# Kernel tuning notes

Measured on AMD Instinct MI355X. Metric: run time of the kernel, lower is better.

Reference implementation:

```python
import jax, jax.numpy as jnp
import numpy as np

B, N, D = 256, 50, 128
NEG = -9e15  # torch uses -9000000000000000.0
LEAKY_SLOPE = 0.2


def setup_inputs() -> dict:
    key = jax.random.key(0)
    ks = jax.random.split(key, 6)
    hidden = jax.random.normal(ks[0], (B, N, D), dtype=jnp.float32)
    adj = jax.random.randint(ks[1], (B, N, N), 0, 5)  # edge types 0..4
    a_0 = jax.random.normal(ks[2], (D, 1), dtype=jnp.float32) * 0.05
    a_1 = jax.random.normal(ks[3], (D, 1), dtype=jnp.float32) * 0.05
    a_2 = jax.random.normal(ks[4], (D, 1), dtype=jnp.float32) * 0.05
    a_3 = jax.random.normal(ks[5], (D, 1), dtype=jnp.float32) * 0.05
    return {"hidden": hidden, "adj": adj, "a_0": a_0, "a_1": a_1, "a_2": a_2, "a_3": a_3}


def reference(hidden, adj, a_0, a_1, a_2, a_3):
    # LocalAggregator.forward (typed-edge GAT over session graph).
    # Original builds a_input[b,i,j,:] = h[b,i,:]*h[b,j,:] (B,N,N,D) then
    # projects with 4 relation vectors a_k (D,1). We fuse: stack the 4
    # vectors and contract D in one einsum -> e[b,k,i,j].
    A = jnp.concatenate([a_0, a_1, a_2, a_3], axis=1)          # (D, 4)
    e = jnp.einsum('bid,bjd,dk->bkij', hidden, hidden, A)      # (B, 4, N, N)
    e = jax.nn.leaky_relu(e, negative_slope=LEAKY_SLOPE)
    # Per-edge-type masking: adj value v in {1..4} selects branch v-1,
    # anything else gets -9e15 (same chained torch.where semantics/order).
    scores = jnp.full_like(e[:, 0], NEG)                        # (B, N, N)
    scores = jnp.where(adj == 1, e[:, 0], scores)
    scores = jnp.where(adj == 2, e[:, 1], scores)
    scores = jnp.where(adj == 3, e[:, 2], scores)
    scores = jnp.where(adj == 4, e[:, 3], scores)
    attn = jax.nn.softmax(scores, axis=-1)                      # (B, N, N)
    return jnp.einsum('bij,bjd->bid', attn, hidden)             # (B, N, D)
```

## Files before the change

### kernel.cpp

```cpp
#include <hip/hip_runtime.h>
#include <stdint.h>

typedef __attribute__((ext_vector_type(8))) short short8;
typedef __attribute__((ext_vector_type(4))) float f32x4;

namespace {
constexpr int   kN     = 50;
constexpr int   kD     = 128;
constexpr float kNeg   = -9.0e15f;
constexpr float kSlope = 0.2f;
constexpr int   HS16   = 136;
constexpr int   ADS    = 52;
constexpr int   HTW    = 66;
constexpr int   PW     = 72;
}

union Pack8 { uint32_t u[4]; short8 s; };

__device__ __forceinline__ uint32_t pack_hl(float v) {
    const uint32_t b  = __float_as_uint(v);
    const uint32_t hi = b & 0xffff0000u;
    const float    r  = v - __uint_as_float(hi);
    return (b >> 16) | (__float_as_uint(r) & 0xffff0000u);
}

__global__ __launch_bounds__(512)
void gat_v13_kernel(const float* __restrict__ hidden,
                    const int*   __restrict__ adj,
                    const float* __restrict__ a0,
                    const float* __restrict__ a1,
                    const float* __restrict__ a2,
                    const float* __restrict__ a3,
                    float* __restrict__ out)
{
    __shared__ unsigned short Hhi[64 * HS16];
    __shared__ unsigned short Hlo[64 * HS16];
    __shared__ uint32_t       Hti[128 * HTW];
    __shared__ unsigned char  Ad [kN * ADS];
    __shared__ float          Xch[8][64][16];
    __shared__ unsigned short Pw2[8][16 * PW];

    const int b    = blockIdx.x;
    const int tid  = threadIdx.x;
    const int lane = tid & 63;
    const int wid  = __builtin_amdgcn_readfirstlane(tid >> 6);
    const int g    = lane >> 4;
    const int f    = lane & 15;

    const float* __restrict__ hb   = hidden + (size_t)b * (kN * kD);
    const int*   __restrict__ adjb = adj    + (size_t)b * (kN * kN);
    float*       __restrict__ outb = out    + (size_t)b * (kN * kD);

    const float4* hg = reinterpret_cast<const float4*>(hb);
    #pragma unroll
    for (int it4 = 0; it4 < 4; ++it4) {
        const int idx = tid + it4 * 512;
        const int j   = idx >> 5;
        const int d4  = idx & 31;
        float4 v = make_float4(0.f, 0.f, 0.f, 0.f);
        if (j < kN) v = hg[j * 32 + d4];

        const uint32_t h0 = __float_as_uint(v.x) & 0xffff0000u;
        const uint32_t h1 = __float_as_uint(v.y) & 0xffff0000u;
        const uint32_t h2 = __float_as_uint(v.z) & 0xffff0000u;
        const uint32_t h3 = __float_as_uint(v.w) & 0xffff0000u;
        uint2 hiw;
        hiw.x = h1 | (h0 >> 16);
        hiw.y = h3 | (h2 >> 16);
        const float r0 = v.x - __uint_as_float(h0);
        const float r1 = v.y - __uint_as_float(h1);
        const float r2 = v.z - __uint_as_float(h2);
        const float r3 = v.w - __uint_as_float(h3);
        uint2 low;
        low.x = (__float_as_uint(r1) & 0xffff0000u) | (__float_as_uint(r0) >> 16);
        low.y = (__float_as_uint(r3) & 0xffff0000u) | (__float_as_uint(r2) >> 16);
        *reinterpret_cast<uint2*>(&Hhi[j * HS16 + 4 * d4]) = hiw;
        *reinterpret_cast<uint2*>(&Hlo[j * HS16 + 4 * d4]) = low;
    }
    for (int idx = tid; idx < 625; idx += 512) {
        const int4 v = reinterpret_cast<const int4*>(adjb)[idx];
        const int e = 4 * idx;
        const int vv[4] = {v.x, v.y, v.z, v.w};
        #pragma unroll
        for (int p = 0; p < 4; ++p) {
            const int ee  = e + p;
            const int row = ee / kN;
            const int col = ee - kN * row;
            Ad[row * ADS + col] = (unsigned char)vv[p];
        }
    }
    const float2* hb2 = reinterpret_cast<const float2*>(hb);
    float2 tv0[4], tv1[4];
    #pragma unroll
    for (int it4 = 0; it4 < 4; ++it4) {
        const int jp = wid + 8 * it4;
        const int j0 = 2 * jp, j1 = 2 * jp + 1;
        tv0[it4] = (j0 < kN) ? hb2[j0 * 64 + lane] : make_float2(0.f, 0.f);
        tv1[it4] = (j1 < kN) ? hb2[j1 * 64 + lane] : make_float2(0.f, 0.f);
    }
    __syncthreads();

    const int it   = wid & 3;
    const int kh   = wid >> 2;
    const int i0   = 16 * it;
    const int irow = (i0 + f < kN) ? (i0 + f) : (kN - 1);

    int adv[4][4];
    #pragma unroll
    for (int jt = 0; jt < 4; ++jt) {
        const int j = 16 * jt + f;
        #pragma unroll
        for (int reg = 0; reg < 4; ++reg) {
            const int ii  = i0 + 4 * g + reg;
            const int iic = (ii < kN) ? ii : (kN - 1);
            adv[jt][reg] = (j < kN) ? (int)Ad[iic * ADS + j] : 0;
        }
    }

    f32x4 acc[4][4];
    #pragma unroll
    for (int jt = 0; jt < 4; ++jt)
        #pragma unroll
        for (int k = 0; k < 4; ++k) acc[jt][k] = (f32x4){0.f, 0.f, 0.f, 0.f};

    const float* __restrict__ aks[4] = {a0, a1, a2, a3};

    #pragma unroll
    for (int ksl2 = 0; ksl2 < 2; ++ksl2) {
        const int dofs = 64 * kh + 32 * ksl2 + 8 * g;

        const short8 ah8 = *reinterpret_cast<const short8*>(&Hhi[irow * HS16 + dofs]);
        const short8 al8 = *reinterpret_cast<const short8*>(&Hlo[irow * HS16 + dofs]);
        float ha[8];
        #pragma unroll
        for (int p = 0; p < 8; ++p) {
            const uint32_t uh = ((uint32_t)(unsigned short)ah8[p]) << 16;
            const uint32_t ul = ((uint32_t)(unsigned short)al8[p]) << 16;
            ha[p] = __uint_as_float(uh) + __uint_as_float(ul);
        }

        short8 qh[4], ql[4];
        #pragma unroll
        for (int k = 0; k < 4; ++k) {
            const float4 av0 = *reinterpret_cast<const float4*>(aks[k] + dofs);
            const float4 av1 = *reinterpret_cast<const float4*>(aks[k] + dofs + 4);
            const float aa[8] = {av0.x, av0.y, av0.z, av0.w, av1.x, av1.y, av1.z, av1.w};
            Pack8 ph, pl;
            #pragma unroll
            for (int p = 0; p < 4; ++p) {
                const float q0 = ha[2 * p]     * aa[2 * p];
                const float q1 = ha[2 * p + 1] * aa[2 * p + 1];
                const uint32_t b0 = __float_as_uint(q0) & 0xffff0000u;
                const uint32_t b1 = __float_as_uint(q1) & 0xffff0000u;
                ph.u[p] = b1 | (b0 >> 16);
                const float s0 = q0 - __uint_as_float(b0);
                const float s1 = q1 - __uint_as_float(b1);
                pl.u[p] = (__float_as_uint(s1) & 0xffff0000u) | (__float_as_uint(s0) >> 16);
            }
            qh[k] = ph.s;
            ql[k] = pl.s;
        }

        #pragma unroll
        for (int jt = 0; jt < 4; ++jt) {
            const int jrow = 16 * jt + f;
            const short8 bh = *reinterpret_cast<const short8*>(&Hhi[jrow * HS16 + dofs]);
            const short8 bl = *reinterpret_cast<const short8*>(&Hlo[jrow * HS16 + dofs]);
            #pragma unroll
            for (int k = 0; k < 4; ++k) {
                acc[jt][k] = __builtin_amdgcn_mfma_f32_16x16x32_bf16(qh[k], bh, acc[jt][k], 0, 0, 0);
                acc[jt][k] = __builtin_amdgcn_mfma_f32_16x16x32_bf16(qh[k], bl, acc[jt][k], 0, 0, 0);
                acc[jt][k] = __builtin_amdgcn_mfma_f32_16x16x32_bf16(ql[k], bh, acc[jt][k], 0, 0, 0);
            }
        }
    }

    f32x4 spart[4];
    uint32_t vmask = 0;
    #pragma unroll
    for (int jt = 0; jt < 4; ++jt) {
        #pragma unroll
        for (int reg = 0; reg < 4; ++reg) {
            const int kv = adv[jt][reg];
            const bool valid = (kv >= 1) && (kv <= 4);
            spart[jt][reg] = (kv == 1) ? acc[jt][0][reg]
                           : (kv == 2) ? acc[jt][1][reg]
                           : (kv == 3) ? acc[jt][2][reg]
                           : (kv == 4) ? acc[jt][3][reg] : 0.f;
            vmask |= (valid ? 1u : 0u) << (4 * jt + reg);
        }
    }

    #pragma unroll
    for (int it4 = 0; it4 < 4; ++it4) {
        const int jp = wid + 8 * it4;
        const int j0 = 2 * jp;
        const int d2 = lane;
        uint2 wa, wb;
        wa.x = pack_hl(tv0[it4].x); wa.y = pack_hl(tv1[it4].x);
        wb.x = pack_hl(tv0[it4].y); wb.y = pack_hl(tv1[it4].y);
        *reinterpret_cast<uint2*>(&Hti[(2 * d2 + 0) * HTW + j0]) = wa;
        *reinterpret_cast<uint2*>(&Hti[(2 * d2 + 1) * HTW + j0]) = wb;
    }

    #pragma unroll
    for (int jt = 0; jt < 4; ++jt)
        *reinterpret_cast<f32x4*>(&Xch[wid][lane][4 * jt]) = spart[jt];
    __syncthreads();

    float s[4][4];
    #pragma unroll
    for (int jt = 0; jt < 4; ++jt) {
        const f32x4 o = *reinterpret_cast<const f32x4*>(&Xch[wid ^ 4][lane][4 * jt]);
        #pragma unroll
        for (int reg = 0; reg < 4; ++reg) {
            const float x  = spart[jt][reg] + o[reg];
            const float lx = (x > 0.f) ? x : kSlope * x;
            s[jt][reg] = ((vmask >> (4 * jt + reg)) & 1u) ? lx : kNeg;
        }
    }

    #pragma unroll
    for (int reg = 0; reg < 4; ++reg) {
        float m = fmaxf(fmaxf(s[0][reg], s[1][reg]), fmaxf(s[2][reg], s[3][reg]));
        #pragma unroll
        for (int o = 1; o < 16; o <<= 1) m = fmaxf(m, __shfl_xor(m, o));

        float e[4];
        float t = 0.f;
        #pragma unroll
        for (int jt = 0; jt < 4; ++jt) {
            const int j = 16 * jt + f;
            e[jt] = (j < kN) ? __expf(s[jt][reg] - m) : 0.f;
            t += e[jt];
        }
        #pragma unroll
        for (int o = 1; o < 16; o <<= 1) t += __shfl_xor(t, o);

        const float inv = 1.0f / t;
        #pragma unroll
        for (int jt = 0; jt < 4; ++jt) {
            uint32_t u = __float_as_uint(e[jt] * inv);
            u += 0x7fffu + ((u >> 16) & 1u);
            Pw2[wid][(4 * g + reg) * PW + 16 * jt + f] = (unsigned short)(u >> 16);
        }
    }

    {
        const int db = 64 * kh;

        const short8 af0 = *reinterpret_cast<const short8*>(&Pw2[wid][f * PW + 0  + 8 * g]);
        const short8 af1 = *reinterpret_cast<const short8*>(&Pw2[wid][f * PW + 32 + 8 * g]);

        f32x4 acc2[4];
        #pragma unroll
        for (int dt = 0; dt < 4; ++dt) acc2[dt] = (f32x4){0.f, 0.f, 0.f, 0.f};

        #pragma unroll
        for (int dt = 0; dt < 4; ++dt) {
            const int drow = db + 16 * dt + f;
            #pragma unroll
            for (int jc = 0; jc < 2; ++jc) {
                const uint32_t* hp = &Hti[drow * HTW + 32 * jc + 8 * g];
                const uint2 u01 = *reinterpret_cast<const uint2*>(hp + 0);
                const uint2 u23 = *reinterpret_cast<const uint2*>(hp + 2);
                const uint2 u45 = *reinterpret_cast<const uint2*>(hp + 4);
                const uint2 u67 = *reinterpret_cast<const uint2*>(hp + 6);
                Pack8 bh, bl;
                bh.u[0] = (u01.x & 0xffffu) | (u01.y << 16);
                bl.u[0] = (u01.x >> 16)     | (u01.y & 0xffff0000u);
                bh.u[1] = (u23.x & 0xffffu) | (u23.y << 16);
                bl.u[1] = (u23.x >> 16)     | (u23.y & 0xffff0000u);
                bh.u[2] = (u45.x & 0xffffu) | (u45.y << 16);
                bl.u[2] = (u45.x >> 16)     | (u45.y & 0xffff0000u);
                bh.u[3] = (u67.x & 0xffffu) | (u67.y << 16);
                bl.u[3] = (u67.x >> 16)     | (u67.y & 0xffff0000u);
                const short8 a8 = jc ? af1 : af0;
                acc2[dt] = __builtin_amdgcn_mfma_f32_16x16x32_bf16(a8, bh.s, acc2[dt], 0, 0, 0);
                acc2[dt] = __builtin_amdgcn_mfma_f32_16x16x32_bf16(a8, bl.s, acc2[dt], 0, 0, 0);
            }
        }

        #pragma unroll
        for (int reg = 0; reg < 4; ++reg) {
            const int ii = 16 * it + 4 * g + reg;
            if (ii < kN) {
                #pragma unroll
                for (int dt = 0; dt < 4; ++dt)
                    outb[ii * kD + db + 16 * dt + f] = acc2[dt][reg];
            }
        }
    }
}

extern "C" void kernel_launch(void* const* d_in, const int* in_sizes, int n_in,
                              void* d_out, int out_size, void* d_ws, size_t ws_size,
                              hipStream_t stream) {
    const float* hidden = reinterpret_cast<const float*>(d_in[0]);
    const int*   adjp   = reinterpret_cast<const int*>(d_in[1]);
    const float* a0     = reinterpret_cast<const float*>(d_in[2]);
    const float* a1     = reinterpret_cast<const float*>(d_in[3]);
    const float* a2     = reinterpret_cast<const float*>(d_in[4]);
    const float* a3     = reinterpret_cast<const float*>(d_in[5]);
    float*       outp   = reinterpret_cast<float*>(d_out);

    gat_v13_kernel<<<dim3(256), dim3(512), 0, stream>>>(
        hidden, adjp, a0, a1, a2, a3, outp);
}
```

Baseline: 16.08 us.

## Warp-specialize into score and transpose waves with 1024-thread blocks

Doubles the block to 16 waves. Waves 0-7 compute the attention scores with MFMA while waves 8-15 load hidden and build the transposed hi/lo copy used by the second matmul, so those two stages run at the same time. The final attn·H product is then split across all 16 waves, each doing half the D columns. This adds an extra barrier and raises register pressure under a 1024-thread launch bound, which could cause spills. It also pads the exchange buffer stride to reduce LDS bank conflicts.

```diff
diff --git a/kernel.cpp b/kernel.cpp
--- a/kernel.cpp
+++ b/kernel.cpp
@@ -13,6 +13,7 @@
 constexpr int   ADS    = 52;
 constexpr int   HTW    = 66;
 constexpr int   PW     = 72;
+constexpr int   XS     = 20;
 }
 
 union Pack8 { uint32_t u[4]; short8 s; };
@@ -24,8 +25,8 @@
     return (b >> 16) | (__float_as_uint(r) & 0xffff0000u);
 }
 
-__global__ __launch_bounds__(512)
-void gat_v13_kernel(const float* __restrict__ hidden,
+__global__ __launch_bounds__(1024)
+void gat_v14_kernel(const float* __restrict__ hidden,
                     const int*   __restrict__ adj,
                     const float* __restrict__ a0,
                     const float* __restrict__ a1,
@@ -37,7 +38,7 @@
     __shared__ unsigned short Hlo[64 * HS16];
     __shared__ uint32_t       Hti[128 * HTW];
     __shared__ unsigned char  Ad [kN * ADS];
-    __shared__ float          Xch[8][64][16];
+    __shared__ float          Xch[8][64][XS];
     __shared__ unsigned short Pw2[8][16 * PW];
 
     const int b    = blockIdx.x;
@@ -46,6 +47,7 @@
     const int wid  = __builtin_amdgcn_readfirstlane(tid >> 6);
     const int g    = lane >> 4;
     const int f    = lane & 15;
+    const bool isScore = (wid < 8);
 
     const float* __restrict__ hb   = hidden + (size_t)b * (kN * kD);
     const int*   __restrict__ adjb = adj    + (size_t)b * (kN * kN);
@@ -53,8 +55,8 @@
 
     const float4* hg = reinterpret_cast<const float4*>(hb);
     #pragma unroll
-    for (int it4 = 0; it4 < 4; ++it4) {
-        const int idx = tid + it4 * 512;
+    for (int it2 = 0; it2 < 2; ++it2) {
+        const int idx = tid + it2 * 1024;
         const int j   = idx >> 5;
         const int d4  = idx & 31;
         float4 v = make_float4(0.f, 0.f, 0.f, 0.f);
@@ -77,9 +79,9 @@
         *reinterpret_cast<uint2*>(&Hhi[j * HS16 + 4 * d4]) = hiw;
         *reinterpret_cast<uint2*>(&Hlo[j * HS16 + 4 * d4]) = low;
     }
-    for (int idx = tid; idx < 625; idx += 512) {
-        const int4 v = reinterpret_cast<const int4*>(adjb)[idx];
-        const int e = 4 * idx;
+    if (tid < 625) {
+        const int4 v = reinterpret_cast<const int4*>(adjb)[tid];
+        const int e = 4 * tid;
         const int vv[4] = {v.x, v.y, v.z, v.w};
         #pragma unroll
         for (int p = 0; p < 4; ++p) {
@@ -91,173 +93,188 @@
     }
     const float2* hb2 = reinterpret_cast<const float2*>(hb);
     float2 tv0[4], tv1[4];
-    #pragma unroll
-    for (int it4 = 0; it4 < 4; ++it4) {
-        const int jp = wid + 8 * it4;
-        const int j0 = 2 * jp, j1 = 2 * jp + 1;
-        tv0[it4] = (j0 < kN) ? hb2[j0 * 64 + lane] : make_float2(0.f, 0.f);
-        tv1[it4] = (j1 < kN) ? hb2[j1 * 64 + lane] : make_float2(0.f, 0.f);
+    if (!isScore) {
+        const int hw = wid - 8;
+        #pragma unroll
+        for (int it4 = 0; it4 < 4; ++it4) {
+            const int jp = hw + 8 * it4;
+            const int j0 = 2 * jp, j1 = 2 * jp + 1;
+            tv0[it4] = (j0 < kN) ? hb2[j0 * 64 + lane] : make_float2(0.f, 0.f);
+            tv1[it4] = (j1 < kN) ? hb2[j1 * 64 + lane] : make_float2(0.f, 0.f);
+        }
     }
     __syncthreads();
 
-    const int it   = wid & 3;
-    const int kh   = wid >> 2;
-    const int i0   = 16 * it;
-    const int irow = (i0 + f < kN) ? (i0 + f) : (kN - 1);
-
-    int adv[4][4];
-    #pragma unroll
-    for (int jt = 0; jt < 4; ++jt) {
-        const int j = 16 * jt + f;
-        #pragma unroll
-        for (int reg = 0; reg < 4; ++reg) {
-            const int ii  = i0 + 4 * g + reg;
-            const int iic = (ii < kN) ? ii : (kN - 1);
-            adv[jt][reg] = (j < kN) ? (int)Ad[iic * ADS + j] : 0;
-        }
-    }
-
-    f32x4 acc[4][4];
-    #pragma unroll
-    for (int jt = 0; jt < 4; ++jt)
-        #pragma unroll
-        for (int k = 0; k < 4; ++k) acc[jt][k] = (f32x4){0.f, 0.f, 0.f, 0.f};
-
-    const float* __restrict__ aks[4] = {a0, a1, a2, a3};
-
-    #pragma unroll
-    for (int ksl2 = 0; ksl2 < 2; ++ksl2) {
-        const int dofs = 64 * kh + 32 * ksl2 + 8 * g;
-
-        const short8 ah8 = *reinterpret_cast<const short8*>(&Hhi[irow * HS16 + dofs]);
-        const short8 al8 = *reinterpret_cast<const short8*>(&Hlo[irow * HS16 + dofs]);
-        float ha[8];
-        #pragma unroll
-        for (int p = 0; p < 8; ++p) {
-            const uint32_t uh = ((uint32_t)(unsigned short)ah8[p]) << 16;
-            const uint32_t ul = ((uint32_t)(unsigned short)al8[p]) << 16;
-            ha[p] = __uint_as_float(uh) + __uint_as_float(ul);
-        }
-
-        short8 qh[4], ql[4];
-        #pragma unroll
-        for (int k = 0; k < 4; ++k) {
-            const float4 av0 = *reinterpret_cast<const float4*>(aks[k] + dofs);
-            const float4 av1 = *reinterpret_cast<const float4*>(aks[k] + dofs + 4);
-            const float aa[8] = {av0.x, av0.y, av0.z, av0.w, av1.x, av1.y, av1.z, av1.w};
-            Pack8 ph, pl;
-            #pragma unroll
-            for (int p = 0; p < 4; ++p) {
-                const float q0 = ha[2 * p]     * aa[2 * p];
-                const float q1 = ha[2 * p + 1] * aa[2 * p + 1];
-                const uint32_t b0 = __float_as_uint(q0) & 0xffff0000u;
-                const uint32_t b1 = __float_as_uint(q1) & 0xffff0000u;
-                ph.u[p] = b1 | (b0 >> 16);
-                const float s0 = q0 - __uint_as_float(b0);
-                const float s1 = q1 - __uint_as_float(b1);
-                pl.u[p] = (__float_as_uint(s1) & 0xffff0000u) | (__float_as_uint(s0) >> 16);
-            }
-            qh[k] = ph.s;
-            ql[k] = pl.s;
-        }
-
-        #pragma unroll
-        for (int jt = 0; jt < 4; ++jt) {
-            const int jrow = 16 * jt + f;
-            const short8 bh = *reinterpret_cast<const short8*>(&Hhi[jrow * HS16 + dofs]);
-            const short8 bl = *reinterpret_cast<const short8*>(&Hlo[jrow * HS16 + dofs]);
-            #pragma unroll
-            for (int k = 0; k < 4; ++k) {
-                acc[jt][k] = __builtin_amdgcn_mfma_f32_16x16x32_bf16(qh[k], bh, acc[jt][k], 0, 0, 0);
-                acc[jt][k] = __builtin_amdgcn_mfma_f32_16x16x32_bf16(qh[k], bl, acc[jt][k], 0, 0, 0);
-                acc[jt][k] = __builtin_amdgcn_mfma_f32_16x16x32_bf16(ql[k], bh, acc[jt][k], 0, 0, 0);
-            }
-        }
-    }
+    const int it = wid & 3;
+    const int kh = (wid >> 2) & 1;
+    const int i0 = 16 * it;
 
     f32x4 spart[4];
     uint32_t vmask = 0;
-    #pragma unroll
-    for (int jt = 0; jt < 4; ++jt) {
-        #pragma unroll
-        for (int reg = 0; reg < 4; ++reg) {
-            const int kv = adv[jt][reg];
-            const bool valid = (kv >= 1) && (kv <= 4);
-            spart[jt][reg] = (kv == 1) ? acc[jt][0][reg]
-                           : (kv == 2) ? acc[jt][1][reg]
-                           : (kv == 3) ? acc[jt][2][reg]
-                           : (kv == 4) ? acc[jt][3][reg] : 0.f;
-            vmask |= (valid ? 1u : 0u) << (4 * jt + reg);
-        }
-    }
-
-    #pragma unroll
-    for (int it4 = 0; it4 < 4; ++it4) {
-        const int jp = wid + 8 * it4;
-        const int j0 = 2 * jp;
-        const int d2 = lane;
-        uint2 wa, wb;
-        wa.x = pack_hl(tv0[it4].x); wa.y = pack_hl(tv1[it4].x);
-        wb.x = pack_hl(tv0[it4].y); wb.y = pack_hl(tv1[it4].y);
-        *reinterpret_cast<uint2*>(&Hti[(2 * d2 + 0) * HTW + j0]) = wa;
-        *reinterpret_cast<uint2*>(&Hti[(2 * d2 + 1) * HTW + j0]) = wb;
-    }
-
-    #pragma unroll
-    for (int jt = 0; jt < 4; ++jt)
-        *reinterpret_cast<f32x4*>(&Xch[wid][lane][4 * jt]) = spart[jt];
-    __syncthreads();
-
-    float s[4][4];
-    #pragma unroll
-    for (int jt = 0; jt < 4; ++jt) {
-        const f32x4 o = *reinterpret_cast<const f32x4*>(&Xch[wid ^ 4][lane][4 * jt]);
-        #pragma unroll
-        for (int reg = 0; reg < 4; ++reg) {
-            const float x  = spart[jt][reg] + o[reg];
-            const float lx = (x > 0.f) ? x : kSlope * x;
-            s[jt][reg] = ((vmask >> (4 * jt + reg)) & 1u) ? lx : kNeg;
-        }
-    }
-
-    #pragma unroll
-    for (int reg = 0; reg < 4; ++reg) {
-        float m = fmaxf(fmaxf(s[0][reg], s[1][reg]), fmaxf(s[2][reg], s[3][reg]));
-        #pragma unroll
-        for (int o = 1; o < 16; o <<= 1) m = fmaxf(m, __shfl_xor(m, o));
-
-        float e[4];
-        float t = 0.f;
+
+    if (isScore) {
+        const int irow = (i0 + f < kN) ? (i0 + f) : (kN - 1);
+
+        uint32_t adv[4];
         #pragma unroll
         for (int jt = 0; jt < 4; ++jt) {
             const int j = 16 * jt + f;
-            e[jt] = (j < kN) ? __expf(s[jt][reg] - m) : 0.f;
-            t += e[jt];
-        }
-        #pragma unroll
-        for (int o = 1; o < 16; o <<= 1) t += __shfl_xor(t, o);
-
-        const float inv = 1.0f / t;
+            uint32_t w = 0;
+            #pragma unroll
+            for (int reg = 0; reg < 4; ++reg) {
+                const int ii  = i0 + 4 * g + reg;
+                const int iic = (ii < kN) ? ii : (kN - 1);
+                const uint32_t kv = (j < kN) ? (uint32_t)Ad[iic * ADS + j] : 0u;
+                w |= kv << (8 * reg);
+            }
+            adv[jt] = w;
+        }
+
+        f32x4 acc[4][4];
+        #pragma unroll
+        for (int jt = 0; jt < 4; ++jt)
+            #pragma unroll
+            for (int k = 0; k < 4; ++k) acc[jt][k] = (f32x4){0.f, 0.f, 0.f, 0.f};
+
+        const float* __restrict__ aks[4] = {a0, a1, a2, a3};
+
+        #pragma unroll
+        for (int ksl2 = 0; ksl2 < 2; ++ksl2) {
+            const int dofs = 64 * kh + 32 * ksl2 + 8 * g;
+
+            const short8 ah8 = *reinterpret_cast<const short8*>(&Hhi[irow * HS16 + dofs]);
+            const short8 al8 = *reinterpret_cast<const short8*>(&Hlo[irow * HS16 + dofs]);
+            float ha[8];
+            #pragma unroll
+            for (int p = 0; p < 8; ++p) {
+                const uint32_t uh = ((uint32_t)(unsigned short)ah8[p]) << 16;
+                const uint32_t ul = ((uint32_t)(unsigned short)al8[p]) << 16;
+                ha[p] = __uint_as_float(uh) + __uint_as_float(ul);
+            }
+
+            short8 qh[4], ql[4];
+            #pragma unroll
+            for (int k = 0; k < 4; ++k) {
+                const float4 av0 = *reinterpret_cast<const float4*>(aks[k] + dofs);
+                const float4 av1 = *reinterpret_cast<const float4*>(aks[k] + dofs + 4);
+                const float aa[8] = {av0.x, av0.y, av0.z, av0.w, av1.x, av1.y, av1.z, av1.w};
+                Pack8 ph, pl;
+                #pragma unroll
+                for (int p = 0; p < 4; ++p) {
+                    const float q0 = ha[2 * p]     * aa[2 * p];
+                    const float q1 = ha[2 * p + 1] * aa[2 * p + 1];
+                    const uint32_t b0 = __float_as_uint(q0) & 0xffff0000u;
+                    const uint32_t b1 = __float_as_uint(q1) & 0xffff0000u;
+                    ph.u[p] = b1 | (b0 >> 16);
+                    const float s0 = q0 - __uint_as_float(b0);
+                    const float s1 = q1 - __uint_as_float(b1);
+                    pl.u[p] = (__float_as_uint(s1) & 0xffff0000u) | (__float_as_uint(s0) >> 16);
+                }
+                qh[k] = ph.s;
+                ql[k] = pl.s;
+            }
+
+            #pragma unroll
+            for (int jt = 0; jt < 4; ++jt) {
+                const int jrow = 16 * jt + f;
+                const short8 bh = *reinterpret_cast<const short8*>(&Hhi[jrow * HS16 + dofs]);
+                const short8 bl = *reinterpret_cast<const short8*>(&Hlo[jrow * HS16 + dofs]);
+                #pragma unroll
+                for (int k = 0; k < 4; ++k) {
+                    acc[jt][k] = __builtin_amdgcn_mfma_f32_16x16x32_bf16(qh[k], bh, acc[jt][k], 0, 0, 0);
+                    acc[jt][k] = __builtin_amdgcn_mfma_f32_16x16x32_bf16(qh[k], bl, acc[jt][k], 0, 0, 0);
+                    acc[jt][k] = __builtin_amdgcn_mfma_f32_16x16x32_bf16(ql[k], bh, acc[jt][k], 0, 0, 0);
+                }
+            }
+        }
+
         #pragma unroll
         for (int jt = 0; jt < 4; ++jt) {
-            uint32_t u = __float_as_uint(e[jt] * inv);
-            u += 0x7fffu + ((u >> 16) & 1u);
-            Pw2[wid][(4 * g + reg) * PW + 16 * jt + f] = (unsigned short)(u >> 16);
-        }
-    }
+            #pragma unroll
+            for (int reg = 0; reg < 4; ++reg) {
+                const int kv = (int)((adv[jt] >> (8 * reg)) & 0xffu);
+                const bool valid = (kv >= 1) && (kv <= 4);
+                spart[jt][reg] = (kv == 1) ? acc[jt][0][reg]
+                               : (kv == 2) ? acc[jt][1][reg]
+                               : (kv == 3) ? acc[jt][2][reg]
+                               : (kv == 4) ? acc[jt][3][reg] : 0.f;
+                vmask |= (valid ? 1u : 0u) << (4 * jt + reg);
+            }
+        }
+
+        #pragma unroll
+        for (int jt = 0; jt < 4; ++jt)
+            *reinterpret_cast<f32x4*>(&Xch[wid][lane][4 * jt]) = spart[jt];
+    } else {
+        #pragma unroll
+        for (int it4 = 0; it4 < 4; ++it4) {
+            const int jp = (wid - 8) + 8 * it4;
+            const int j0 = 2 * jp;
+            const int d2 = lane;
+            uint2 wa, wb;
+            wa.x = pack_hl(tv0[it4].x); wa.y = pack_hl(tv1[it4].x);
+            wb.x = pack_hl(tv0[it4].y); wb.y = pack_hl(tv1[it4].y);
+            *reinterpret_cast<uint2*>(&Hti[(2 * d2 + 0) * HTW + j0]) = wa;
+            *reinterpret_cast<uint2*>(&Hti[(2 * d2 + 1) * HTW + j0]) = wb;
+        }
+    }
+    __syncthreads();
+
+    if (isScore) {
+        float s[4][4];
+        #pragma unroll
+        for (int jt = 0; jt < 4; ++jt) {
+            const f32x4 o = *reinterpret_cast<const f32x4*>(&Xch[wid ^ 4][lane][4 * jt]);
+            #pragma unroll
+            for (int reg = 0; reg < 4; ++reg) {
+                const float x  = spart[jt][reg] + o[reg];
+                const float lx = (x > 0.f) ? x : kSlope * x;
+                s[jt][reg] = ((vmask >> (4 * jt + reg)) & 1u) ? lx : kNeg;
+            }
+        }
+
+        #pragma unroll
+        for (int reg = 0; reg < 4; ++reg) {
+            float m = fmaxf(fmaxf(s[0][reg], s[1][reg]), fmaxf(s[2][reg], s[3][reg]));
+            #pragma unroll
+            for (int o = 1; o < 16; o <<= 1) m = fmaxf(m, __shfl_xor(m, o));
+
+            float e[4];
+            float t = 0.f;
+            #pragma unroll
+            for (int jt = 0; jt < 4; ++jt) {
+                const int j = 16 * jt + f;
+                e[jt] = (j < kN) ? __expf(s[jt][reg] - m) : 0.f;
+                t += e[jt];
+            }
+            #pragma unroll
+            for (int o = 1; o < 16; o <<= 1) t += __shfl_xor(t, o);
+
+            const float inv = 1.0f / t;
+            #pragma unroll
+            for (int jt = 0; jt < 4; ++jt) {
+                uint32_t u = __float_as_uint(e[jt] * inv);
+                u += 0x7fffu + ((u >> 16) & 1u);
+                Pw2[wid][(4 * g + reg) * PW + 16 * jt + f] = (unsigned short)(u >> 16);
+            }
+        }
+    }
+    __syncthreads();
 
     {
-        const int db = 64 * kh;
-
-        const short8 af0 = *reinterpret_cast<const short8*>(&Pw2[wid][f * PW + 0  + 8 * g]);
-        const short8 af1 = *reinterpret_cast<const short8*>(&Pw2[wid][f * PW + 32 + 8 * g]);
-
-        f32x4 acc2[4];
-        #pragma unroll
-        for (int dt = 0; dt < 4; ++dt) acc2[dt] = (f32x4){0.f, 0.f, 0.f, 0.f};
-
-        #pragma unroll
-        for (int dt = 0; dt < 4; ++dt) {
+        const int dq  = wid >> 2;
+        const int db  = 32 * dq;
+        const int src = it + 4 * (dq & 1);
+
+        const short8 af0 = *reinterpret_cast<const short8*>(&Pw2[src][f * PW + 0  + 8 * g]);
+        const short8 af1 = *reinterpret_cast<const short8*>(&Pw2[src][f * PW + 32 + 8 * g]);
+
+        f32x4 acc2[2];
+        acc2[0] = (f32x4){0.f, 0.f, 0.f, 0.f};
+        acc2[1] = acc2[0];
+
+        #pragma unroll
+        for (int dt = 0; dt < 2; ++dt) {
             const int drow = db + 16 * dt + f;
             #pragma unroll
             for (int jc = 0; jc < 2; ++jc) {
@@ -283,10 +300,10 @@
 
         #pragma unroll
         for (int reg = 0; reg < 4; ++reg) {
-            const int ii = 16 * it + 4 * g + reg;
+            const int ii = i0 + 4 * g + reg;
             if (ii < kN) {
                 #pragma unroll
-                for (int dt = 0; dt < 4; ++dt)
+                for (int dt = 0; dt < 2; ++dt)
                     outb[ii * kD + db + 16 * dt + f] = acc2[dt][reg];
             }
         }
@@ -304,6 +321,6 @@
     const float* a3     = reinterpret_cast<const float*>(d_in[5]);
     float*       outp   = reinterpret_cast<float*>(d_out);
 
-    gat_v13_kernel<<<dim3(256), dim3(512), 0, stream>>>(
+    gat_v14_kernel<<<dim3(256), dim3(1024), 0, stream>>>(
         hidden, adjp, a0, a1, a2, a3, outp);
 }
```

After: 20.61 us. +28.1%, slower.
